# Performance work log

Measured on AMD Instinct MI355X. Metric: run time of the kernel, lower is better.

Reference implementation:

```python
import jax, jax.numpy as jnp
import numpy as np

B, L, V, D = 4096, 128, 50257, 64
NEG_INF = -1e9
COS_EPS = 1e-8  # torch cosine_similarity default eps


def setup_inputs() -> dict:
    key = jax.random.key(0)
    k1, k2, k3, k4, k5, k6 = jax.random.split(key, 6)
    return {
        "ids_a": jax.random.randint(k1, (B, L), 0, V, dtype=jnp.int64) if jax.config.jax_enable_x64 else jax.random.randint(k1, (B, L), 0, V, dtype=jnp.int32),
        "mask_a": jax.random.randint(k2, (B, L), 0, 2, dtype=jnp.int32),
        "ids_b": jax.random.randint(k3, (B, L), 0, V, dtype=jnp.int32),
        "mask_b": jax.random.randint(k4, (B, L), 0, 2, dtype=jnp.int32),
        "mu_table": jax.random.normal(k5, (V, D), dtype=jnp.float32),
        "feat_table": jax.random.normal(k6, (V, D), dtype=jnp.float32),
    }


def _side(ids, mask, mu_table, feat_table):
    # Embedding gathers: [B, L, D]
    mu = mu_table[ids]
    feat = feat_table[ids]
    m = mask.astype(mu.dtype)  # [B, L]
    # render_mean_pool: masked mean of mu -> query [B, D]
    denom = jnp.maximum(m.sum(axis=1, keepdims=True), 1.0)
    q = jnp.einsum('bld,bl->bd', mu, m) / denom
    # render_softmax_attention: single-query masked softmax over mu keys
    scores = jnp.einsum('bld,bd->bl', mu, q)
    scores = jnp.where(mask.astype(bool), scores, NEG_INF)
    attn = jax.nn.softmax(scores, axis=-1)  # [B, L]
    return jnp.einsum('bl,bld->bd', attn, feat)  # weighted sum of feat


def reference(ids_a, mask_a, ids_b, mask_b, mu_table, feat_table):
    mean_a = _side(ids_a, mask_a, mu_table, feat_table)
    mean_b = _side(ids_b, mask_b, mu_table, feat_table)
    # torch cosine_similarity: x.y / (max(||x||, eps) * max(||y||, eps))
    na = jnp.maximum(jnp.linalg.norm(mean_a, axis=-1), COS_EPS)
    nb = jnp.maximum(jnp.linalg.norm(mean_b, axis=-1), COS_EPS)
    cos = jnp.sum(mean_a * mean_b, axis=-1) / (na * nb)
    return cos * 5.0
```

## Files before the change

kernel.cpp:

```cpp
#include <hip/hip_runtime.h>
#include <hip/hip_fp16.h>
#include <math.h>

#define BB 4096
#define LL 128
#define DD 64
#define VV 50257
#define TAB_ELEMS (VV * DD)

typedef _Float16 h2_t __attribute__((ext_vector_type(2)));

__device__ __forceinline__ float dot2acc(unsigned a, unsigned b, float c) {
#if __has_builtin(__builtin_amdgcn_fdot2)
    return __builtin_amdgcn_fdot2(__builtin_bit_cast(h2_t, a),
                                  __builtin_bit_cast(h2_t, b), c, false);
#else
    const float2 fa = __half22float2(*(const __half2*)&a);
    const float2 fb = __half22float2(*(const __half2*)&b);
    return fmaf(fa.x, fb.x, fmaf(fa.y, fb.y, c));
#endif
}

__device__ __forceinline__ float2 cvt2(unsigned raw) {
    return __half22float2(*(const __half2*)&raw);
}

__device__ __forceinline__ unsigned pack_h2(float a, float b) {
    union { __half2 h; unsigned u; } p;
    p.h = __floats2half2_rn(a, b);
    return p.u;
}

__global__ __launch_bounds__(256) void convert_tables_kernel(
    const float* __restrict__ mu, const float* __restrict__ feat,
    __half* __restrict__ out_mu, __half* __restrict__ out_feat)
{
    const int n4 = TAB_ELEMS / 4;
    for (int i = blockIdx.x * blockDim.x + threadIdx.x; i < n4;
         i += gridDim.x * blockDim.x) {
        const float4 m = ((const float4*)mu)[i];
        const float4 f = ((const float4*)feat)[i];
        uint2 pm, pf;
        pm.x = pack_h2(m.x, m.y); pm.y = pack_h2(m.z, m.w);
        pf.x = pack_h2(f.x, f.y); pf.y = pack_h2(f.z, f.w);
        ((uint2*)out_mu)[i]   = pm;
        ((uint2*)out_feat)[i] = pf;
    }
}

__global__ __launch_bounds__(256, 6) void softmax_attn_cos_kernel(
    const int* __restrict__ ids_a, const int* __restrict__ mask_a,
    const int* __restrict__ ids_b, const int* __restrict__ mask_b,
    const __half* __restrict__ mu_table, const __half* __restrict__ feat_table,
    float* __restrict__ out)
{
    __shared__ int      s_ids[2][LL];
    __shared__ float    s_msk[2][LL];
    __shared__ unsigned s_qh[2][32];
    __shared__ float4   s_qp[2][2][16];
    __shared__ float    s_sc[2][LL];
    __shared__ float4   s_op[2][2][16];
    __shared__ float    s_mean[2][DD];
    __shared__ float    s_sum[2];

    const int tid  = threadIdx.x;
    const int lane = tid & 63;
    const int wave = tid >> 6;
    const int side = wave >> 1;
    const int wsub = wave & 1;
    const int r8   = lane >> 3;
    const int c8   = lane & 7;
    const int b    = blockIdx.x;

    {
        const int si = tid >> 7;
        const int l  = tid & 127;
        const int* idp = si ? ids_b  : ids_a;
        const int* mp  = si ? mask_b : mask_a;
        s_ids[si][l] = idp[b * LL + l];
        s_msk[si][l] = (float)mp[b * LL + l];
    }
    __syncthreads();

    uint4 v[8];
    unsigned kept = 0;
    {
        float4 qa = make_float4(0.f, 0.f, 0.f, 0.f);
        float4 qb = make_float4(0.f, 0.f, 0.f, 0.f);
        #pragma unroll
        for (int it = 0; it < 8; ++it) {
            const int r = wsub * 64 + it * 8 + r8;
            if (s_msk[side][r] > 0.5f) {
                kept |= (1u << it);
                v[it] = ((const uint4*)(mu_table + (size_t)s_ids[side][r] * DD))[c8];
                const float2 f0 = cvt2(v[it].x), f1 = cvt2(v[it].y);
                const float2 f2 = cvt2(v[it].z), f3 = cvt2(v[it].w);
                qa.x += f0.x; qa.y += f0.y; qa.z += f1.x; qa.w += f1.y;
                qb.x += f2.x; qb.y += f2.y; qb.z += f3.x; qb.w += f3.y;
            } else {
                v[it] = make_uint4(0u, 0u, 0u, 0u);
            }
        }
        #pragma unroll
        for (int off = 8; off <= 32; off <<= 1) {
            qa.x += __shfl_xor(qa.x, off, 64); qa.y += __shfl_xor(qa.y, off, 64);
            qa.z += __shfl_xor(qa.z, off, 64); qa.w += __shfl_xor(qa.w, off, 64);
            qb.x += __shfl_xor(qb.x, off, 64); qb.y += __shfl_xor(qb.y, off, 64);
            qb.z += __shfl_xor(qb.z, off, 64); qb.w += __shfl_xor(qb.w, off, 64);
        }
        if (lane < 8) {
            s_qp[side][wsub][2 * c8]     = qa;
            s_qp[side][wsub][2 * c8 + 1] = qb;
        }
    }
    __syncthreads();

    if (tid < 128) {
        const int si = tid >> 6;
        const int dd = tid & 63;
        float mv = s_msk[si][dd] + s_msk[si][dd + 64];
        #pragma unroll
        for (int off = 32; off; off >>= 1) mv += __shfl_xor(mv, off, 64);
        const float denom = fmaxf(mv, 1.0f);
        if (dd < 16) {
            const float4 q0 = s_qp[si][0][dd], q1 = s_qp[si][1][dd];
            const float qx = (q0.x + q1.x) / denom, qy = (q0.y + q1.y) / denom;
            const float qz = (q0.z + q1.z) / denom, qw = (q0.w + q1.w) / denom;
            s_qh[si][2 * dd]     = pack_h2(qx, qy);
            s_qh[si][2 * dd + 1] = pack_h2(qz, qw);
        }
    }
    __syncthreads();

    {
        const uint4 qq = ((const uint4*)&s_qh[side][0])[c8];
        #pragma unroll
        for (int it = 0; it < 8; ++it) {
            const int r = wsub * 64 + it * 8 + r8;
            float p = dot2acc(v[it].x, qq.x, 0.f);
            p = dot2acc(v[it].y, qq.y, p);
            p = dot2acc(v[it].z, qq.z, p);
            p = dot2acc(v[it].w, qq.w, p);
            const uint4 nf =
                ((const uint4*)(feat_table + (size_t)s_ids[side][r] * DD))[c8];
            #pragma unroll
            for (int off = 1; off <= 4; off <<= 1)
                p += __shfl_xor(p, off, 64);
            if (c8 == 0) s_sc[side][r] = ((kept >> it) & 1u) ? p : -1e9f;
            v[it] = nf;
        }
    }
    __syncthreads();

    if (wsub == 0) {
        const float s1 = s_sc[side][lane], s2 = s_sc[side][lane + 64];
        float mx = fmaxf(s1, s2);
        #pragma unroll
        for (int off = 32; off; off >>= 1) mx = fmaxf(mx, __shfl_xor(mx, off, 64));
        const float e1 = expf(s1 - mx), e2 = expf(s2 - mx);
        s_sc[side][lane] = e1; s_sc[side][lane + 64] = e2;
        float sm = e1 + e2;
        #pragma unroll
        for (int off = 32; off; off >>= 1) sm += __shfl_xor(sm, off, 64);
        if (lane == 0) s_sum[side] = sm;
    }
    __syncthreads();

    {
        float4 oa = make_float4(0.f, 0.f, 0.f, 0.f);
        float4 ob = make_float4(0.f, 0.f, 0.f, 0.f);
        #pragma unroll
        for (int it = 0; it < 8; ++it) {
            const int r = wsub * 64 + it * 8 + r8;
            const float w = s_sc[side][r];
            const float2 f0 = cvt2(v[it].x), f1 = cvt2(v[it].y);
            const float2 f2 = cvt2(v[it].z), f3 = cvt2(v[it].w);
            oa.x = fmaf(f0.x, w, oa.x); oa.y = fmaf(f0.y, w, oa.y);
            oa.z = fmaf(f1.x, w, oa.z); oa.w = fmaf(f1.y, w, oa.w);
            ob.x = fmaf(f2.x, w, ob.x); ob.y = fmaf(f2.y, w, ob.y);
            ob.z = fmaf(f3.x, w, ob.z); ob.w = fmaf(f3.y, w, ob.w);
        }
        #pragma unroll
        for (int off = 8; off <= 32; off <<= 1) {
            oa.x += __shfl_xor(oa.x, off, 64); oa.y += __shfl_xor(oa.y, off, 64);
            oa.z += __shfl_xor(oa.z, off, 64); oa.w += __shfl_xor(oa.w, off, 64);
            ob.x += __shfl_xor(ob.x, off, 64); ob.y += __shfl_xor(ob.y, off, 64);
            ob.z += __shfl_xor(ob.z, off, 64); ob.w += __shfl_xor(ob.w, off, 64);
        }
        if (lane < 8) {
            s_op[side][wsub][2 * c8]     = oa;
            s_op[side][wsub][2 * c8 + 1] = ob;
        }
    }
    __syncthreads();

    if (tid < 32) {
        const int si = tid >> 4, cc = tid & 15;
        const float inv = 1.0f / s_sum[si];
        const float4 o0 = s_op[si][0][cc], o1 = s_op[si][1][cc];
        float4 o;
        o.x = (o0.x + o1.x) * inv; o.y = (o0.y + o1.y) * inv;
        o.z = (o0.z + o1.z) * inv; o.w = (o0.w + o1.w) * inv;
        ((float4*)&s_mean[si][0])[cc] = o;
    }
    __syncthreads();

    if (tid < 64) {
        const float a = s_mean[0][tid], c = s_mean[1][tid];
        float dt = a * c, na = a * a, nb = c * c;
        #pragma unroll
        for (int off = 32; off; off >>= 1) {
            dt += __shfl_xor(dt, off, 64);
            na += __shfl_xor(na, off, 64);
            nb += __shfl_xor(nb, off, 64);
        }
        if (tid == 0) {
            const float denom = fmaxf(sqrtf(na), 1e-8f) * fmaxf(sqrtf(nb), 1e-8f);
            out[b] = 5.0f * dt / denom;
        }
    }
}

extern "C" void kernel_launch(void* const* d_in, const int* in_sizes, int n_in,
                              void* d_out, int out_size, void* d_ws, size_t ws_size,
                              hipStream_t stream) {
    const int*   ids_a  = (const int*)d_in[0];
    const int*   mask_a = (const int*)d_in[1];
    const int*   ids_b  = (const int*)d_in[2];
    const int*   mask_b = (const int*)d_in[3];
    const float* mu     = (const float*)d_in[4];
    const float* feat   = (const float*)d_in[5];
    float* out = (float*)d_out;

    __half* ws_mu   = (__half*)d_ws;
    __half* ws_feat = ws_mu + TAB_ELEMS;

    convert_tables_kernel<<<1024, 256, 0, stream>>>(mu, feat, ws_mu, ws_feat);
    softmax_attn_cos_kernel<<<BB, 256, 0, stream>>>(
        ids_a, mask_a, ids_b, mask_b, ws_mu, ws_feat, out);
}
```

Measured before the change: 114.0 us.

## Drop two block barriers and skip feat gathers for masked tokens

```diff
diff --git a/kernel.cpp b/kernel.cpp
--- a/kernel.cpp
+++ b/kernel.cpp
@@ -54,14 +54,12 @@
     const __half* __restrict__ mu_table, const __half* __restrict__ feat_table,
     float* __restrict__ out)
 {
-    __shared__ int      s_ids[2][LL];
-    __shared__ float    s_msk[2][LL];
-    __shared__ unsigned s_qh[2][32];
-    __shared__ float4   s_qp[2][2][16];
-    __shared__ float    s_sc[2][LL];
-    __shared__ float4   s_op[2][2][16];
-    __shared__ float    s_mean[2][DD];
-    __shared__ float    s_sum[2];
+    __shared__ int    s_ids[2][LL];
+    __shared__ float  s_msk[2][LL];
+    __shared__ float4 s_qp[2][2][16];
+    __shared__ float  s_sc[2][LL];
+    __shared__ float4 s_op[2][2][16];
+    __shared__ float  s_sum[2];
 
     const int tid  = threadIdx.x;
     const int lane = tid & 63;
@@ -81,6 +79,12 @@
         s_msk[si][l] = (float)mp[b * LL + l];
     }
     __syncthreads();
+
+    float mv = s_msk[side][lane] + s_msk[side][lane + 64];
+    #pragma unroll
+    for (int off = 32; off; off >>= 1) mv += __shfl_xor(mv, off, 64);
+    const float denom = fmaxf(mv, 1.0f);
+    const bool  allm  = (mv < 0.5f);
 
     uint4 v[8];
     unsigned kept = 0;
@@ -115,25 +119,16 @@
     }
     __syncthreads();
 
-    if (tid < 128) {
-        const int si = tid >> 6;
-        const int dd = tid & 63;
-        float mv = s_msk[si][dd] + s_msk[si][dd + 64];
-        #pragma unroll
-        for (int off = 32; off; off >>= 1) mv += __shfl_xor(mv, off, 64);
-        const float denom = fmaxf(mv, 1.0f);
-        if (dd < 16) {
-            const float4 q0 = s_qp[si][0][dd], q1 = s_qp[si][1][dd];
-            const float qx = (q0.x + q1.x) / denom, qy = (q0.y + q1.y) / denom;
-            const float qz = (q0.z + q1.z) / denom, qw = (q0.w + q1.w) / denom;
-            s_qh[si][2 * dd]     = pack_h2(qx, qy);
-            s_qh[si][2 * dd + 1] = pack_h2(qz, qw);
-        }
-    }
-    __syncthreads();
-
-    {
-        const uint4 qq = ((const uint4*)&s_qh[side][0])[c8];
+    {
+        const float rd = 1.0f / denom;
+        const float4 p00 = s_qp[side][0][2 * c8], p01 = s_qp[side][0][2 * c8 + 1];
+        const float4 p10 = s_qp[side][1][2 * c8], p11 = s_qp[side][1][2 * c8 + 1];
+        uint4 qq;
+        qq.x = pack_h2((p00.x + p10.x) * rd, (p00.y + p10.y) * rd);
+        qq.y = pack_h2((p00.z + p10.z) * rd, (p00.w + p10.w) * rd);
+        qq.z = pack_h2((p01.x + p11.x) * rd, (p01.y + p11.y) * rd);
+        qq.w = pack_h2((p01.z + p11.z) * rd, (p01.w + p11.w) * rd);
+
         #pragma unroll
         for (int it = 0; it < 8; ++it) {
             const int r = wsub * 64 + it * 8 + r8;
@@ -141,8 +136,9 @@
             p = dot2acc(v[it].y, qq.y, p);
             p = dot2acc(v[it].z, qq.z, p);
             p = dot2acc(v[it].w, qq.w, p);
-            const uint4 nf =
-                ((const uint4*)(feat_table + (size_t)s_ids[side][r] * DD))[c8];
+            uint4 nf = make_uint4(0u, 0u, 0u, 0u);
+            if (allm || ((kept >> it) & 1u))
+                nf = ((const uint4*)(feat_table + (size_t)s_ids[side][r] * DD))[c8];
             #pragma unroll
             for (int off = 1; off <= 4; off <<= 1)
                 p += __shfl_xor(p, off, 64);
@@ -194,19 +190,15 @@
     }
     __syncthreads();
 
-    if (tid < 32) {
-        const int si = tid >> 4, cc = tid & 15;
-        const float inv = 1.0f / s_sum[si];
-        const float4 o0 = s_op[si][0][cc], o1 = s_op[si][1][cc];
-        float4 o;
-        o.x = (o0.x + o1.x) * inv; o.y = (o0.y + o1.y) * inv;
-        o.z = (o0.z + o1.z) * inv; o.w = (o0.w + o1.w) * inv;
-        ((float4*)&s_mean[si][0])[cc] = o;
-    }
-    __syncthreads();
-
     if (tid < 64) {
-        const float a = s_mean[0][tid], c = s_mean[1][tid];
+        const float inva = 1.0f / s_sum[0];
+        const float invb = 1.0f / s_sum[1];
+        const float* pa0 = (const float*)&s_op[0][0][0];
+        const float* pa1 = (const float*)&s_op[0][1][0];
+        const float* pb0 = (const float*)&s_op[1][0][0];
+        const float* pb1 = (const float*)&s_op[1][1][0];
+        const float a = (pa0[tid] + pa1[tid]) * inva;
+        const float c = (pb0[tid] + pb1[tid]) * invb;
         float dt = a * c, na = a * a, nb = c * c;
         #pragma unroll
         for (int off = 32; off; off >>= 1) {
@@ -215,8 +207,8 @@
             nb += __shfl_xor(nb, off, 64);
         }
         if (tid == 0) {
-            const float denom = fmaxf(sqrtf(na), 1e-8f) * fmaxf(sqrtf(nb), 1e-8f);
-            out[b] = 5.0f * dt / denom;
+            const float dn = fmaxf(sqrtf(na), 1e-8f) * fmaxf(sqrtf(nb), 1e-8f);
+            out[b] = 5.0f * dt / dn;
         }
     }
 }
```

Result: no change. 115.2 us (+1.0%).
